# Performance work log

Hardware: AMD Instinct MI355X
Metric: run time of the kernel (lower is better)

The kernel has to match this reference:

```python
import jax, jax.numpy as jnp
import numpy as np

N_NODES = 100000
N_EDGES = 1600000
IN_DIM = 128
HID = 64


def _init_linear(key, fan_in, fan_out):
    kw, kb = jax.random.split(key)
    bound = 1.0 / np.sqrt(fan_in)
    W = jax.random.uniform(kw, (fan_in, fan_out), jnp.float32, -bound, bound)
    b = jax.random.uniform(kb, (fan_out,), jnp.float32, -bound, bound)
    return W, b


def setup_inputs() -> dict:
    key = jax.random.key(0)
    ks = jax.random.split(key, 6)
    x = jax.random.normal(ks[0], (N_NODES, IN_DIM), jnp.float32)
    edge_index = jax.random.randint(ks[1], (2, N_EDGES), 0, N_NODES, jnp.int64)
    W_pre, b_pre = _init_linear(ks[2], IN_DIM, HID)
    W1, b1 = _init_linear(ks[3], HID, HID)
    W2, b2 = _init_linear(ks[4], HID, HID)
    W3, b3 = _init_linear(ks[5], HID, HID)
    return {"x": x, "edge_index": edge_index, "W_pre": W_pre, "b_pre": b_pre,
            "W1": W1, "b1": b1, "W2": W2, "b2": b2, "W3": W3, "b3": b3}


def _gcn_layer(h, src, dst, dinv, W, b):
    # PyG GCNConv: h' = D^{-1/2} (A + I) D^{-1/2} (h W) + b, deg from A+I
    n = h.shape[0]
    hw = h @ W                                  # [N, out]
    norm = dinv[src] * dinv[dst]                # [E]
    msg = hw[src] * norm[:, None]               # gather + scale  [E, out]
    agg = jax.ops.segment_sum(msg, dst, num_segments=n)  # scatter-add
    agg = agg + hw * (dinv * dinv)[:, None]     # self-loop term (norm = dinv_i^2)
    return agg + b


def reference(x, edge_index, W_pre, b_pre, W1, b1, W2, b2, W3, b3):
    src, dst = edge_index[0], edge_index[1]
    n = x.shape[0]
    # degree of A + I (self loops added, as in GCNConv default)
    deg = jax.ops.segment_sum(jnp.ones(src.shape[0], x.dtype), dst, num_segments=n) + 1.0
    dinv = jax.lax.rsqrt(deg)

    h = x @ W_pre + b_pre                       # feature_pre linear
    h = jax.nn.relu(_gcn_layer(h, src, dst, dinv, W1, b1))  # dropout is identity in eval
    h = jax.nn.relu(_gcn_layer(h, src, dst, dinv, W2, b2))
    h = _gcn_layer(h, src, dst, dinv, W3, b3)
    # F.normalize(p=2, dim=-1) with eps=1e-12
    nrm = jnp.linalg.norm(h, axis=-1, keepdims=True)
    return h / jnp.maximum(nrm, 1e-12)
```

## Files before the change

kernel.cpp:

```cpp
#include <hip/hip_runtime.h>
#include <hip/hip_bf16.h>

#define N_NODES 100000
#define N_EDGES 1600000
#define IN_DIM 128
#define HID 64
#define NB 782

typedef __attribute__((ext_vector_type(8))) _Float16 h8v;
typedef __attribute__((ext_vector_type(4))) float f4v;

__global__ __launch_bounds__(256) void k_bhist(const int* __restrict__ dst,
                                               int* __restrict__ bsz) {
  __shared__ int cnt[NB];
  for (int b = threadIdx.x; b < NB; b += 256) cnt[b] = 0;
  __syncthreads();
  int e0 = blockIdx.x * 8192;
  int eend = min(e0 + 8192, N_EDGES);
  for (int e = e0 + threadIdx.x; e < eend; e += 256)
    atomicAdd(&cnt[dst[e] >> 7], 1);
  __syncthreads();
  for (int b = threadIdx.x; b < NB; b += 256)
    if (cnt[b]) atomicAdd(&bsz[b], cnt[b]);
}

__global__ __launch_bounds__(1024) void k_bscan(const int* __restrict__ bsz,
                                                int* __restrict__ bboff,
                                                int* __restrict__ bcur) {
  __shared__ int sc[1024];
  int t = threadIdx.x;
  int v = (t < NB) ? bsz[t] : 0;
  sc[t] = v;
  __syncthreads();
  for (int off = 1; off < 1024; off <<= 1) {
    int u = (t >= off) ? sc[t - off] : 0;
    __syncthreads();
    sc[t] += u;
    __syncthreads();
  }
  if (t < NB) {
    int excl = sc[t] - v;
    bboff[t] = excl;
    bcur[t] = excl;
    if (t == NB - 1) bboff[NB] = excl + v;
  }
}

__global__ __launch_bounds__(256) void k_partition(const int* __restrict__ ei,
                                                   int* __restrict__ bcur,
                                                   int2* __restrict__ pairs) {
  __shared__ int cnt[NB];
  __shared__ int base[NB];
  for (int b = threadIdx.x; b < NB; b += 256) cnt[b] = 0;
  __syncthreads();
  int e0 = blockIdx.x * 8192;
  int eend = min(e0 + 8192, N_EDGES);
  for (int e = e0 + threadIdx.x; e < eend; e += 256) {
    int d = ei[N_EDGES + e];
    atomicAdd(&cnt[d >> 7], 1);
  }
  __syncthreads();
  for (int b = threadIdx.x; b < NB; b += 256) {
    int c = cnt[b];
    base[b] = c ? atomicAdd(&bcur[b], c) : 0;
    cnt[b] = 0;
  }
  __syncthreads();
  for (int e = e0 + threadIdx.x; e < eend; e += 256) {
    int s = ei[e];
    int d = ei[N_EDGES + e];
    int b = d >> 7;
    int r = atomicAdd(&cnt[b], 1);
    pairs[base[b] + r] = make_int2(s, d);
  }
}

__global__ __launch_bounds__(256) void k_csr_deg(const int2* __restrict__ pairs,
                                                 const int* __restrict__ bboff,
                                                 int* __restrict__ offs,
                                                 float* __restrict__ dinv,
                                                 int* __restrict__ csr) {
  __shared__ int ldeg[128];
  __shared__ int sc[128];
  __shared__ int lcur[128];
  int t = threadIdx.x;
  int node0 = blockIdx.x << 7;
  int nloc = min(128, N_NODES - node0);
  int beg = bboff[blockIdx.x];
  int end = bboff[blockIdx.x + 1];
  if (t < 128) ldeg[t] = 0;
  __syncthreads();
  for (int i = beg + t; i < end; i += 256)
    atomicAdd(&ldeg[pairs[i].y - node0], 1);
  __syncthreads();
  int dv = (t < 128) ? ldeg[t] : 0;
  if (t < 128) sc[t] = dv;
  __syncthreads();
  for (int off = 1; off < 128; off <<= 1) {
    int u = (t >= off && t < 128) ? sc[t - off] : 0;
    __syncthreads();
    if (t < 128) sc[t] += u;
    __syncthreads();
  }
  if (t < nloc) {
    int excl = sc[t] - dv;
    int o = beg + excl;
    offs[node0 + t] = o;
    lcur[t] = o;
    dinv[node0 + t] = rsqrtf((float)dv + 1.0f);
  }
  if (blockIdx.x == NB - 1 && t == 0) offs[N_NODES] = N_EDGES;
  __syncthreads();
  for (int i = beg + t; i < end; i += 256) {
    int2 p = pairs[i];
    int pos = atomicAdd(&lcur[p.y - node0], 1);
    csr[pos] = p.x;
  }
}

__device__ __forceinline__ void split_one(const float* W, _Float16* hi, _Float16* lo,
                                          int K, int i) {
  int k = i >> 6, n = i & 63;
  float v = W[i];
  _Float16 h = (_Float16)v;
  float r = v - (float)h;
  hi[n * K + k] = h;
  lo[n * K + k] = (_Float16)r;
}

__global__ __launch_bounds__(256) void k_prep_all(
    const float* __restrict__ Wp, const float* __restrict__ W1,
    const float* __restrict__ W2, const float* __restrict__ W3,
    _Float16* __restrict__ WpH, _Float16* __restrict__ WpL,
    _Float16* __restrict__ W1H, _Float16* __restrict__ W1L,
    _Float16* __restrict__ W2H, _Float16* __restrict__ W2L,
    _Float16* __restrict__ W3H, _Float16* __restrict__ W3L) {
  int blk = blockIdx.x;
  if (blk < 32) split_one(Wp, WpH, WpL, IN_DIM, blk * 256 + threadIdx.x);
  else if (blk < 48) split_one(W1, W1H, W1L, HID, (blk - 32) * 256 + threadIdx.x);
  else if (blk < 64) split_one(W2, W2H, W2L, HID, (blk - 48) * 256 + threadIdx.x);
  else split_one(W3, W3H, W3L, HID, (blk - 64) * 256 + threadIdx.x);
}

template <int K, bool BIAS, typename OutT>
__global__ __launch_bounds__(256) void k_gemm_mfma(const float* __restrict__ X,
                                                   const _Float16* __restrict__ Wh,
                                                   const _Float16* __restrict__ Wl,
                                                   const float* __restrict__ bias,
                                                   OutT* __restrict__ out) {
  int wave = threadIdx.x >> 6;
  int lane = threadIdx.x & 63;
  int fi = lane & 15;
  int quad = lane >> 4;
  int r0 = blockIdx.x * 64 + wave * 16;
  int row_l = r0 + fi;
  if (row_l >= N_NODES) row_l = N_NODES - 1;
  const float* xp = X + (size_t)row_l * K + quad * 8;

  f4v acc[4];
#pragma unroll
  for (int ct = 0; ct < 4; ++ct) acc[ct] = (f4v){0.f, 0.f, 0.f, 0.f};

#pragma unroll
  for (int k0 = 0; k0 < K; k0 += 32) {
    f4v xa = *(const f4v*)(xp + k0);
    f4v xb = *(const f4v*)(xp + k0 + 4);
    h8v ah, al;
#pragma unroll
    for (int j = 0; j < 4; ++j) {
      _Float16 h = (_Float16)xa[j];
      ah[j] = h;
      al[j] = (_Float16)(xa[j] - (float)h);
    }
#pragma unroll
    for (int j = 0; j < 4; ++j) {
      _Float16 h = (_Float16)xb[j];
      ah[4 + j] = h;
      al[4 + j] = (_Float16)(xb[j] - (float)h);
    }
    const _Float16* whp = Wh + (size_t)fi * K + k0 + quad * 8;
    const _Float16* wlp = Wl + (size_t)fi * K + k0 + quad * 8;
#pragma unroll
    for (int ct = 0; ct < 4; ++ct) {
      h8v bh = *(const h8v*)(whp + (size_t)ct * 16 * K);
      h8v bl = *(const h8v*)(wlp + (size_t)ct * 16 * K);
      acc[ct] = __builtin_amdgcn_mfma_f32_16x16x32_f16(ah, bh, acc[ct], 0, 0, 0);
      acc[ct] = __builtin_amdgcn_mfma_f32_16x16x32_f16(al, bh, acc[ct], 0, 0, 0);
      acc[ct] = __builtin_amdgcn_mfma_f32_16x16x32_f16(ah, bl, acc[ct], 0, 0, 0);
    }
  }

#pragma unroll
  for (int ct = 0; ct < 4; ++ct) {
    float bv = 0.f;
    if (BIAS) bv = bias[ct * 16 + fi];
#pragma unroll
    for (int j = 0; j < 4; ++j) {
      int orow = r0 + quad * 4 + j;
      if (orow < N_NODES) out[(size_t)orow * HID + ct * 16 + fi] = (OutT)(acc[ct][j] + bv);
    }
  }
}

template <int MODE>
__global__ __launch_bounds__(256) void k_agg(const _Float16* __restrict__ hw,
                                             const int* __restrict__ offs,
                                             const int* __restrict__ csr,
                                             const float* __restrict__ dinv,
                                             const float* __restrict__ bias,
                                             float* __restrict__ out) {
  int node = blockIdx.x * 4 + (threadIdx.x >> 6);
  int lane = threadIdx.x & 63;
  int oct = lane >> 3;
  int fi = lane & 7;
  float di = dinv[node];
  int beg = offs[node];
  int end = offs[node + 1];

  float acc[8];
#pragma unroll
  for (int c = 0; c < 8; ++c) acc[c] = 0.f;

  if (oct == 0) {
    h8v hv = *(const h8v*)(hw + (size_t)node * HID + fi * 8);
    float w = di * di;
#pragma unroll
    for (int c = 0; c < 8; ++c) acc[c] += (float)hv[c] * w;
  }
  for (int e0 = beg + oct; e0 < end; e0 += 16) {
    int ss[2];
    float ww[2];
#pragma unroll
    for (int j = 0; j < 2; ++j) {
      int e = e0 + 8 * j;
      bool v = e < end;
      int s = csr[v ? e : beg];
      ss[j] = v ? s : node;
      ww[j] = v ? di : 0.0f;
    }
#pragma unroll
    for (int j = 0; j < 2; ++j) ww[j] *= dinv[ss[j]];
    h8v hv[2];
#pragma unroll
    for (int j = 0; j < 2; ++j)
      hv[j] = *(const h8v*)(hw + (size_t)ss[j] * HID + fi * 8);
#pragma unroll
    for (int j = 0; j < 2; ++j)
#pragma unroll
      for (int c = 0; c < 8; ++c) acc[c] += (float)hv[j][c] * ww[j];
  }
#pragma unroll
  for (int c = 0; c < 8; ++c) {
    float v = acc[c];
    v += __shfl_xor(v, 8);
    v += __shfl_xor(v, 16);
    v += __shfl_xor(v, 32);
    acc[c] = v;
  }
  if (oct == 0) {
#pragma unroll
    for (int c = 0; c < 8; ++c) acc[c] += bias[fi * 8 + c];
    if (MODE == 0) {
#pragma unroll
      for (int c = 0; c < 8; ++c) acc[c] = fmaxf(acc[c], 0.f);
    } else {
      float ss = 0.f;
#pragma unroll
      for (int c = 0; c < 8; ++c) ss += acc[c] * acc[c];
      ss += __shfl_xor(ss, 1);
      ss += __shfl_xor(ss, 2);
      ss += __shfl_xor(ss, 4);
      float sc = 1.0f / fmaxf(sqrtf(ss), 1e-12f);
#pragma unroll
      for (int c = 0; c < 8; ++c) acc[c] *= sc;
    }
    f4v o0 = {acc[0], acc[1], acc[2], acc[3]};
    f4v o1 = {acc[4], acc[5], acc[6], acc[7]};
    *(f4v*)(out + (size_t)node * HID + fi * 8) = o0;
    *(f4v*)(out + (size_t)node * HID + fi * 8 + 4) = o1;
  }
}

extern "C" void kernel_launch(void* const* d_in, const int* in_sizes, int n_in,
                              void* d_out, int out_size, void* d_ws, size_t ws_size,
                              hipStream_t stream) {
  const float* x     = (const float*)d_in[0];
  const int*   ei    = (const int*)d_in[1];
  const float* W_pre = (const float*)d_in[2];
  const float* b_pre = (const float*)d_in[3];
  const float* W1    = (const float*)d_in[4];
  const float* b1    = (const float*)d_in[5];
  const float* W2    = (const float*)d_in[6];
  const float* b2    = (const float*)d_in[7];
  const float* W3    = (const float*)d_in[8];
  const float* b3    = (const float*)d_in[9];
  float* out = (float*)d_out;

  char* ws = (char*)d_ws;
  float*    bufA  = (float*)(ws + 0);
  int2*     pairs = (int2*)(ws + 0);
  _Float16* hw16  = (_Float16*)(ws + 25600000);
  int*      csr   = (int*)(ws + 38400000);
  int*      offs  = (int*)(ws + 44800000);
  float*    dinv  = (float*)(ws + 45200016);
  int*      bsz   = (int*)(ws + 45600016);
  int*      bboff = (int*)(ws + 45603200);
  int*      bcur  = (int*)(ws + 45606400);
  _Float16* WpreH = (_Float16*)(ws + 45610000);
  _Float16* WpreL = (_Float16*)(ws + 45626384);
  _Float16* W1H   = (_Float16*)(ws + 45642768);
  _Float16* W1L   = (_Float16*)(ws + 45650960);
  _Float16* W2H   = (_Float16*)(ws + 45659152);
  _Float16* W2L   = (_Float16*)(ws + 45667344);
  _Float16* W3H   = (_Float16*)(ws + 45675536);
  _Float16* W3L   = (_Float16*)(ws + 45683728);

  const int GEMM_BLOCKS = (N_NODES + 63) / 64;
  const int PART_BLOCKS = (N_EDGES + 8191) / 8192;

  hipMemsetAsync(bsz, 0, NB * sizeof(int), stream);
  k_bhist<<<PART_BLOCKS, 256, 0, stream>>>(ei + N_EDGES, bsz);
  k_bscan<<<1, 1024, 0, stream>>>(bsz, bboff, bcur);
  k_partition<<<PART_BLOCKS, 256, 0, stream>>>(ei, bcur, pairs);
  k_csr_deg<<<NB, 256, 0, stream>>>(pairs, bboff, offs, dinv, csr);

  k_prep_all<<<80, 256, 0, stream>>>(W_pre, W1, W2, W3, WpreH, WpreL,
                                     W1H, W1L, W2H, W2L, W3H, W3L);

  k_gemm_mfma<IN_DIM, true, float><<<GEMM_BLOCKS, 256, 0, stream>>>(x, WpreH, WpreL, b_pre, bufA);

  k_gemm_mfma<HID, false, _Float16><<<GEMM_BLOCKS, 256, 0, stream>>>(bufA, W1H, W1L, nullptr, hw16);
  k_agg<0><<<N_NODES / 4, 256, 0, stream>>>(hw16, offs, csr, dinv, b1, bufA);
  k_gemm_mfma<HID, false, _Float16><<<GEMM_BLOCKS, 256, 0, stream>>>(bufA, W2H, W2L, nullptr, hw16);
  k_agg<0><<<N_NODES / 4, 256, 0, stream>>>(hw16, offs, csr, dinv, b2, bufA);
  k_gemm_mfma<HID, false, _Float16><<<GEMM_BLOCKS, 256, 0, stream>>>(bufA, W3H, W3L, nullptr, hw16);
  k_agg<1><<<N_NODES / 4, 256, 0, stream>>>(hw16, offs, csr, dinv, b3, out);
}
```

Measured before the change: 386.1 us.

## Fuse whole GCN pipeline into one cooperative persistent kernel with grid syncs

```diff
diff --git a/kernel.cpp b/kernel.cpp
--- a/kernel.cpp
+++ b/kernel.cpp
@@ -1,125 +1,44 @@
 #include <hip/hip_runtime.h>
-#include <hip/hip_bf16.h>
+#include <hip/hip_cooperative_groups.h>
+
+namespace cg = cooperative_groups;
 
 #define N_NODES 100000
 #define N_EDGES 1600000
 #define IN_DIM 128
 #define HID 64
 #define NB 782
+#define NT64 1563
+#define NGROUP 25000
+#define MAXGRID 2048
 
 typedef __attribute__((ext_vector_type(8))) _Float16 h8v;
 typedef __attribute__((ext_vector_type(4))) float f4v;
 
-__global__ __launch_bounds__(256) void k_bhist(const int* __restrict__ dst,
-                                               int* __restrict__ bsz) {
-  __shared__ int cnt[NB];
-  for (int b = threadIdx.x; b < NB; b += 256) cnt[b] = 0;
-  __syncthreads();
-  int e0 = blockIdx.x * 8192;
-  int eend = min(e0 + 8192, N_EDGES);
-  for (int e = e0 + threadIdx.x; e < eend; e += 256)
-    atomicAdd(&cnt[dst[e] >> 7], 1);
-  __syncthreads();
-  for (int b = threadIdx.x; b < NB; b += 256)
-    if (cnt[b]) atomicAdd(&bsz[b], cnt[b]);
-}
-
-__global__ __launch_bounds__(1024) void k_bscan(const int* __restrict__ bsz,
-                                                int* __restrict__ bboff,
-                                                int* __restrict__ bcur) {
-  __shared__ int sc[1024];
-  int t = threadIdx.x;
-  int v = (t < NB) ? bsz[t] : 0;
-  sc[t] = v;
-  __syncthreads();
-  for (int off = 1; off < 1024; off <<= 1) {
-    int u = (t >= off) ? sc[t - off] : 0;
-    __syncthreads();
-    sc[t] += u;
-    __syncthreads();
-  }
-  if (t < NB) {
-    int excl = sc[t] - v;
-    bboff[t] = excl;
-    bcur[t] = excl;
-    if (t == NB - 1) bboff[NB] = excl + v;
-  }
-}
-
-__global__ __launch_bounds__(256) void k_partition(const int* __restrict__ ei,
-                                                   int* __restrict__ bcur,
-                                                   int2* __restrict__ pairs) {
-  __shared__ int cnt[NB];
-  __shared__ int base[NB];
-  for (int b = threadIdx.x; b < NB; b += 256) cnt[b] = 0;
-  __syncthreads();
-  int e0 = blockIdx.x * 8192;
-  int eend = min(e0 + 8192, N_EDGES);
-  for (int e = e0 + threadIdx.x; e < eend; e += 256) {
-    int d = ei[N_EDGES + e];
-    atomicAdd(&cnt[d >> 7], 1);
-  }
-  __syncthreads();
-  for (int b = threadIdx.x; b < NB; b += 256) {
-    int c = cnt[b];
-    base[b] = c ? atomicAdd(&bcur[b], c) : 0;
-    cnt[b] = 0;
-  }
-  __syncthreads();
-  for (int e = e0 + threadIdx.x; e < eend; e += 256) {
-    int s = ei[e];
-    int d = ei[N_EDGES + e];
-    int b = d >> 7;
-    int r = atomicAdd(&cnt[b], 1);
-    pairs[base[b] + r] = make_int2(s, d);
-  }
-}
-
-__global__ __launch_bounds__(256) void k_csr_deg(const int2* __restrict__ pairs,
-                                                 const int* __restrict__ bboff,
-                                                 int* __restrict__ offs,
-                                                 float* __restrict__ dinv,
-                                                 int* __restrict__ csr) {
-  __shared__ int ldeg[128];
-  __shared__ int sc[128];
-  __shared__ int lcur[128];
-  int t = threadIdx.x;
-  int node0 = blockIdx.x << 7;
-  int nloc = min(128, N_NODES - node0);
-  int beg = bboff[blockIdx.x];
-  int end = bboff[blockIdx.x + 1];
-  if (t < 128) ldeg[t] = 0;
-  __syncthreads();
-  for (int i = beg + t; i < end; i += 256)
-    atomicAdd(&ldeg[pairs[i].y - node0], 1);
-  __syncthreads();
-  int dv = (t < 128) ? ldeg[t] : 0;
-  if (t < 128) sc[t] = dv;
-  __syncthreads();
-  for (int off = 1; off < 128; off <<= 1) {
-    int u = (t >= off && t < 128) ? sc[t - off] : 0;
-    __syncthreads();
-    if (t < 128) sc[t] += u;
-    __syncthreads();
-  }
-  if (t < nloc) {
-    int excl = sc[t] - dv;
-    int o = beg + excl;
-    offs[node0 + t] = o;
-    lcur[t] = o;
-    dinv[node0 + t] = rsqrtf((float)dv + 1.0f);
-  }
-  if (blockIdx.x == NB - 1 && t == 0) offs[N_NODES] = N_EDGES;
-  __syncthreads();
-  for (int i = beg + t; i < end; i += 256) {
-    int2 p = pairs[i];
-    int pos = atomicAdd(&lcur[p.y - node0], 1);
-    csr[pos] = p.x;
-  }
-}
-
-__device__ __forceinline__ void split_one(const float* W, _Float16* hi, _Float16* lo,
-                                          int K, int i) {
+struct MegaArgs {
+  const float* x; const int* ei;
+  const float* Wp; const float* bp;
+  const float* W1; const float* b1;
+  const float* W2; const float* b2;
+  const float* W3; const float* b3;
+  float* out;
+  float* bufA; _Float16* hw16;
+  int* pairs; int* csr; int* offs; float* dinv;
+  int* bsz; int* bboff; int* bcur;
+  _Float16* WpH; _Float16* WpL; _Float16* W1H; _Float16* W1L;
+  _Float16* W2H; _Float16* W2L; _Float16* W3H; _Float16* W3L;
+};
+
+union SM {
+  int bh[NB];
+  struct { int cnt[NB]; int base[NB]; } part;
+  struct { int ldeg[128]; int sc[128]; int lcur[128]; } cd;
+  int scan[256];
+};
+
+__device__ __forceinline__ void d_split(const float* __restrict__ W,
+                                        _Float16* __restrict__ hi,
+                                        _Float16* __restrict__ lo, int K, int i) {
   int k = i >> 6, n = i & 63;
   float v = W[i];
   _Float16 h = (_Float16)v;
@@ -128,31 +47,17 @@
   lo[n * K + k] = (_Float16)r;
 }
 
-__global__ __launch_bounds__(256) void k_prep_all(
-    const float* __restrict__ Wp, const float* __restrict__ W1,
-    const float* __restrict__ W2, const float* __restrict__ W3,
-    _Float16* __restrict__ WpH, _Float16* __restrict__ WpL,
-    _Float16* __restrict__ W1H, _Float16* __restrict__ W1L,
-    _Float16* __restrict__ W2H, _Float16* __restrict__ W2L,
-    _Float16* __restrict__ W3H, _Float16* __restrict__ W3L) {
-  int blk = blockIdx.x;
-  if (blk < 32) split_one(Wp, WpH, WpL, IN_DIM, blk * 256 + threadIdx.x);
-  else if (blk < 48) split_one(W1, W1H, W1L, HID, (blk - 32) * 256 + threadIdx.x);
-  else if (blk < 64) split_one(W2, W2H, W2L, HID, (blk - 48) * 256 + threadIdx.x);
-  else split_one(W3, W3H, W3L, HID, (blk - 64) * 256 + threadIdx.x);
-}
-
 template <int K, bool BIAS, typename OutT>
-__global__ __launch_bounds__(256) void k_gemm_mfma(const float* __restrict__ X,
-                                                   const _Float16* __restrict__ Wh,
-                                                   const _Float16* __restrict__ Wl,
-                                                   const float* __restrict__ bias,
-                                                   OutT* __restrict__ out) {
+__device__ __forceinline__ void d_gemm(int tile, const float* __restrict__ X,
+                                       const _Float16* __restrict__ Wh,
+                                       const _Float16* __restrict__ Wl,
+                                       const float* __restrict__ bias,
+                                       OutT* __restrict__ out) {
   int wave = threadIdx.x >> 6;
   int lane = threadIdx.x & 63;
   int fi = lane & 15;
   int quad = lane >> 4;
-  int r0 = blockIdx.x * 64 + wave * 16;
+  int r0 = tile * 64 + wave * 16;
   int row_l = r0 + fi;
   if (row_l >= N_NODES) row_l = N_NODES - 1;
   const float* xp = X + (size_t)row_l * K + quad * 8;
@@ -189,7 +94,6 @@
       acc[ct] = __builtin_amdgcn_mfma_f32_16x16x32_f16(ah, bl, acc[ct], 0, 0, 0);
     }
   }
-
 #pragma unroll
   for (int ct = 0; ct < 4; ++ct) {
     float bv = 0.f;
@@ -203,13 +107,13 @@
 }
 
 template <int MODE>
-__global__ __launch_bounds__(256) void k_agg(const _Float16* __restrict__ hw,
-                                             const int* __restrict__ offs,
-                                             const int* __restrict__ csr,
-                                             const float* __restrict__ dinv,
-                                             const float* __restrict__ bias,
-                                             float* __restrict__ out) {
-  int node = blockIdx.x * 4 + (threadIdx.x >> 6);
+__device__ __forceinline__ void d_agg(int grp, const _Float16* __restrict__ hw,
+                                      const int* __restrict__ offs,
+                                      const int* __restrict__ csr,
+                                      const float* __restrict__ dinv,
+                                      const float* __restrict__ bias,
+                                      float* __restrict__ out) {
+  int node = grp * 4 + (threadIdx.x >> 6);
   int lane = threadIdx.x & 63;
   int oct = lane >> 3;
   int fi = lane & 7;
@@ -227,11 +131,11 @@
 #pragma unroll
     for (int c = 0; c < 8; ++c) acc[c] += (float)hv[c] * w;
   }
-  for (int e0 = beg + oct; e0 < end; e0 += 16) {
-    int ss[2];
-    float ww[2];
-#pragma unroll
-    for (int j = 0; j < 2; ++j) {
+  for (int e0 = beg + oct; e0 < end; e0 += 32) {
+    int ss[4];
+    float ww[4];
+#pragma unroll
+    for (int j = 0; j < 4; ++j) {
       int e = e0 + 8 * j;
       bool v = e < end;
       int s = csr[v ? e : beg];
@@ -239,13 +143,13 @@
       ww[j] = v ? di : 0.0f;
     }
 #pragma unroll
-    for (int j = 0; j < 2; ++j) ww[j] *= dinv[ss[j]];
-    h8v hv[2];
-#pragma unroll
-    for (int j = 0; j < 2; ++j)
+    for (int j = 0; j < 4; ++j) ww[j] *= dinv[ss[j]];
+    h8v hv[4];
+#pragma unroll
+    for (int j = 0; j < 4; ++j)
       hv[j] = *(const h8v*)(hw + (size_t)ss[j] * HID + fi * 8);
 #pragma unroll
-    for (int j = 0; j < 2; ++j)
+    for (int j = 0; j < 4; ++j)
 #pragma unroll
       for (int c = 0; c < 8; ++c) acc[c] += (float)hv[j][c] * ww[j];
   }
@@ -281,58 +185,331 @@
   }
 }
 
+__global__ __launch_bounds__(256, 4) void k_mega(MegaArgs a) {
+  cg::grid_group g = cg::this_grid();
+  __shared__ SM sm;
+  int blk = blockIdx.x;
+  int grid = gridDim.x;
+  int t = threadIdx.x;
+
+  if (blk == 0) {
+    for (int i = t; i < NB; i += 256) a.bsz[i] = 0;
+  } else if (blk <= 32) {
+    d_split(a.Wp, a.WpH, a.WpL, IN_DIM, (blk - 1) * 256 + t);
+  } else if (blk <= 48) {
+    d_split(a.W1, a.W1H, a.W1L, HID, (blk - 33) * 256 + t);
+  } else if (blk <= 64) {
+    d_split(a.W2, a.W2H, a.W2L, HID, (blk - 49) * 256 + t);
+  } else if (blk <= 80) {
+    d_split(a.W3, a.W3H, a.W3L, HID, (blk - 65) * 256 + t);
+  }
+  g.sync();
+
+  if (blk < 196) {
+    for (int i = t; i < NB; i += 256) sm.bh[i] = 0;
+    __syncthreads();
+    int e0 = blk * 8192, e1 = min(e0 + 8192, N_EDGES);
+    for (int e = e0 + t; e < e1; e += 256)
+      atomicAdd(&sm.bh[a.ei[N_EDGES + e] >> 7], 1);
+    __syncthreads();
+    for (int i = t; i < NB; i += 256)
+      if (sm.bh[i]) atomicAdd(&a.bsz[i], sm.bh[i]);
+  } else {
+    for (int tile = blk - 196; tile < NT64; tile += grid - 196)
+      d_gemm<IN_DIM, true, float>(tile, a.x, a.WpH, a.WpL, a.bp, a.bufA);
+  }
+  g.sync();
+
+  if (blk == 0) {
+    int c[4];
+    int idx0 = t * 4;
+#pragma unroll
+    for (int j = 0; j < 4; ++j) c[j] = (idx0 + j < NB) ? a.bsz[idx0 + j] : 0;
+    int tsum = c[0] + c[1] + c[2] + c[3];
+    int val = tsum;
+    sm.scan[t] = val;
+    __syncthreads();
+    for (int off = 1; off < 256; off <<= 1) {
+      int u = (t >= off) ? sm.scan[t - off] : 0;
+      __syncthreads();
+      val += u;
+      sm.scan[t] = val;
+      __syncthreads();
+    }
+    int excl = val - tsum;
+#pragma unroll
+    for (int j = 0; j < 4; ++j) {
+      int idx = idx0 + j;
+      if (idx < NB) { a.bboff[idx] = excl; a.bcur[idx] = excl; }
+      excl += c[j];
+    }
+    if (t == 255) a.bboff[NB] = val;
+  }
+  g.sync();
+
+  if (blk < 196) {
+    for (int i = t; i < NB; i += 256) sm.part.cnt[i] = 0;
+    __syncthreads();
+    int e0 = blk * 8192, e1 = min(e0 + 8192, N_EDGES);
+    for (int e = e0 + t; e < e1; e += 256)
+      atomicAdd(&sm.part.cnt[a.ei[N_EDGES + e] >> 7], 1);
+    __syncthreads();
+    for (int i = t; i < NB; i += 256) {
+      int c = sm.part.cnt[i];
+      sm.part.base[i] = c ? atomicAdd(&a.bcur[i], c) : 0;
+      sm.part.cnt[i] = 0;
+    }
+    __syncthreads();
+    for (int e = e0 + t; e < e1; e += 256) {
+      int s = a.ei[e];
+      int d = a.ei[N_EDGES + e];
+      int b = d >> 7;
+      int r = atomicAdd(&sm.part.cnt[b], 1);
+      a.pairs[sm.part.base[b] + r] = ((d & 127) << 17) | s;
+    }
+  }
+  g.sync();
+
+  for (int b = blk; b < NB; b += grid) {
+    int node0 = b << 7;
+    int nloc = min(128, N_NODES - node0);
+    int beg = a.bboff[b], end = a.bboff[b + 1];
+    if (t < 128) sm.cd.ldeg[t] = 0;
+    __syncthreads();
+    for (int i = beg + t; i < end; i += 256)
+      atomicAdd(&sm.cd.ldeg[(a.pairs[i] >> 17) & 127], 1);
+    __syncthreads();
+    int dv = (t < 128) ? sm.cd.ldeg[t] : 0;
+    if (t < 128) sm.cd.sc[t] = dv;
+    __syncthreads();
+    for (int off = 1; off < 128; off <<= 1) {
+      int u = (t >= off && t < 128) ? sm.cd.sc[t - off] : 0;
+      __syncthreads();
+      if (t < 128) sm.cd.sc[t] += u;
+      __syncthreads();
+    }
+    if (t < nloc) {
+      int o = beg + sm.cd.sc[t] - dv;
+      a.offs[node0 + t] = o;
+      sm.cd.lcur[t] = o;
+      a.dinv[node0 + t] = rsqrtf((float)dv + 1.0f);
+    }
+    if (b == NB - 1 && t == 0) a.offs[N_NODES] = N_EDGES;
+    __syncthreads();
+    for (int i = beg + t; i < end; i += 256) {
+      int p = a.pairs[i];
+      int pos = atomicAdd(&sm.cd.lcur[(p >> 17) & 127], 1);
+      a.csr[pos] = p & 131071;
+    }
+    __syncthreads();
+  }
+  g.sync();
+
+  for (int tile = blk; tile < NT64; tile += grid)
+    d_gemm<HID, false, _Float16>(tile, a.bufA, a.W1H, a.W1L, nullptr, a.hw16);
+  g.sync();
+  for (int grp = blk; grp < NGROUP; grp += grid)
+    d_agg<0>(grp, a.hw16, a.offs, a.csr, a.dinv, a.b1, a.bufA);
+  g.sync();
+
+  for (int tile = blk; tile < NT64; tile += grid)
+    d_gemm<HID, false, _Float16>(tile, a.bufA, a.W2H, a.W2L, nullptr, a.hw16);
+  g.sync();
+  for (int grp = blk; grp < NGROUP; grp += grid)
+    d_agg<0>(grp, a.hw16, a.offs, a.csr, a.dinv, a.b2, a.bufA);
+  g.sync();
+
+  for (int tile = blk; tile < NT64; tile += grid)
+    d_gemm<HID, false, _Float16>(tile, a.bufA, a.W3H, a.W3L, nullptr, a.hw16);
+  g.sync();
+  for (int grp = blk; grp < NGROUP; grp += grid)
+    d_agg<1>(grp, a.hw16, a.offs, a.csr, a.dinv, a.b3, a.out);
+}
+
+__global__ __launch_bounds__(256) void f_prep(MegaArgs a) {
+  int blk = blockIdx.x, t = threadIdx.x;
+  if (blk < 32) d_split(a.Wp, a.WpH, a.WpL, IN_DIM, blk * 256 + t);
+  else if (blk < 48) d_split(a.W1, a.W1H, a.W1L, HID, (blk - 32) * 256 + t);
+  else if (blk < 64) d_split(a.W2, a.W2H, a.W2L, HID, (blk - 48) * 256 + t);
+  else d_split(a.W3, a.W3H, a.W3L, HID, (blk - 64) * 256 + t);
+}
+
+__global__ __launch_bounds__(256) void f_bhist(MegaArgs a) {
+  __shared__ int cnt[NB];
+  int t = threadIdx.x;
+  for (int i = t; i < NB; i += 256) cnt[i] = 0;
+  __syncthreads();
+  int e0 = blockIdx.x * 8192, e1 = min(e0 + 8192, N_EDGES);
+  for (int e = e0 + t; e < e1; e += 256)
+    atomicAdd(&cnt[a.ei[N_EDGES + e] >> 7], 1);
+  __syncthreads();
+  for (int i = t; i < NB; i += 256)
+    if (cnt[i]) atomicAdd(&a.bsz[i], cnt[i]);
+}
+
+__global__ __launch_bounds__(256) void f_bscan(MegaArgs a) {
+  __shared__ int sm[256];
+  int t = threadIdx.x;
+  int c[4];
+  int idx0 = t * 4;
+#pragma unroll
+  for (int j = 0; j < 4; ++j) c[j] = (idx0 + j < NB) ? a.bsz[idx0 + j] : 0;
+  int tsum = c[0] + c[1] + c[2] + c[3];
+  int val = tsum;
+  sm[t] = val;
+  __syncthreads();
+  for (int off = 1; off < 256; off <<= 1) {
+    int u = (t >= off) ? sm[t - off] : 0;
+    __syncthreads();
+    val += u;
+    sm[t] = val;
+    __syncthreads();
+  }
+  int excl = val - tsum;
+#pragma unroll
+  for (int j = 0; j < 4; ++j) {
+    int idx = idx0 + j;
+    if (idx < NB) { a.bboff[idx] = excl; a.bcur[idx] = excl; }
+    excl += c[j];
+  }
+  if (t == 255) a.bboff[NB] = val;
+}
+
+__global__ __launch_bounds__(256) void f_partition(MegaArgs a) {
+  __shared__ int cnt[NB];
+  __shared__ int base[NB];
+  int t = threadIdx.x;
+  for (int i = t; i < NB; i += 256) cnt[i] = 0;
+  __syncthreads();
+  int e0 = blockIdx.x * 8192, e1 = min(e0 + 8192, N_EDGES);
+  for (int e = e0 + t; e < e1; e += 256)
+    atomicAdd(&cnt[a.ei[N_EDGES + e] >> 7], 1);
+  __syncthreads();
+  for (int i = t; i < NB; i += 256) {
+    int c = cnt[i];
+    base[i] = c ? atomicAdd(&a.bcur[i], c) : 0;
+    cnt[i] = 0;
+  }
+  __syncthreads();
+  for (int e = e0 + t; e < e1; e += 256) {
+    int s = a.ei[e];
+    int d = a.ei[N_EDGES + e];
+    int b = d >> 7;
+    int r = atomicAdd(&cnt[b], 1);
+    a.pairs[base[b] + r] = ((d & 127) << 17) | s;
+  }
+}
+
+__global__ __launch_bounds__(256) void f_csrdeg(MegaArgs a) {
+  __shared__ int ldeg[128];
+  __shared__ int sc[128];
+  __shared__ int lcur[128];
+  int t = threadIdx.x;
+  int b = blockIdx.x;
+  int node0 = b << 7;
+  int nloc = min(128, N_NODES - node0);
+  int beg = a.bboff[b], end = a.bboff[b + 1];
+  if (t < 128) ldeg[t] = 0;
+  __syncthreads();
+  for (int i = beg + t; i < end; i += 256)
+    atomicAdd(&ldeg[(a.pairs[i] >> 17) & 127], 1);
+  __syncthreads();
+  int dv = (t < 128) ? ldeg[t] : 0;
+  if (t < 128) sc[t] = dv;
+  __syncthreads();
+  for (int off = 1; off < 128; off <<= 1) {
+    int u = (t >= off && t < 128) ? sc[t - off] : 0;
+    __syncthreads();
+    if (t < 128) sc[t] += u;
+    __syncthreads();
+  }
+  if (t < nloc) {
+    int o = beg + sc[t] - dv;
+    a.offs[node0 + t] = o;
+    lcur[t] = o;
+    a.dinv[node0 + t] = rsqrtf((float)dv + 1.0f);
+  }
+  if (b == NB - 1 && t == 0) a.offs[N_NODES] = N_EDGES;
+  __syncthreads();
+  for (int i = beg + t; i < end; i += 256) {
+    int p = a.pairs[i];
+    int pos = atomicAdd(&lcur[(p >> 17) & 127], 1);
+    a.csr[pos] = p & 131071;
+  }
+}
+
+__global__ __launch_bounds__(256) void f_gemm_pre(MegaArgs a) {
+  d_gemm<IN_DIM, true, float>(blockIdx.x, a.x, a.WpH, a.WpL, a.bp, a.bufA);
+}
+
+__global__ __launch_bounds__(256) void f_gemm64(MegaArgs a, const _Float16* Wh,
+                                                const _Float16* Wl) {
+  d_gemm<HID, false, _Float16>(blockIdx.x, a.bufA, Wh, Wl, nullptr, a.hw16);
+}
+
+__global__ __launch_bounds__(256) void f_agg_relu(MegaArgs a, const float* bias) {
+  d_agg<0>(blockIdx.x, a.hw16, a.offs, a.csr, a.dinv, bias, a.bufA);
+}
+
+__global__ __launch_bounds__(256) void f_agg_norm(MegaArgs a) {
+  d_agg<1>(blockIdx.x, a.hw16, a.offs, a.csr, a.dinv, a.b3, a.out);
+}
+
 extern "C" void kernel_launch(void* const* d_in, const int* in_sizes, int n_in,
                               void* d_out, int out_size, void* d_ws, size_t ws_size,
                               hipStream_t stream) {
-  const float* x     = (const float*)d_in[0];
-  const int*   ei    = (const int*)d_in[1];
-  const float* W_pre = (const float*)d_in[2];
-  const float* b_pre = (const float*)d_in[3];
-  const float* W1    = (const float*)d_in[4];
-  const float* b1    = (const float*)d_in[5];
-  const float* W2    = (const float*)d_in[6];
-  const float* b2    = (const float*)d_in[7];
-  const float* W3    = (const float*)d_in[8];
-  const float* b3    = (const float*)d_in[9];
-  float* out = (float*)d_out;
-
   char* ws = (char*)d_ws;
-  float*    bufA  = (float*)(ws + 0);
-  int2*     pairs = (int2*)(ws + 0);
-  _Float16* hw16  = (_Float16*)(ws + 25600000);
-  int*      csr   = (int*)(ws + 38400000);
-  int*      offs  = (int*)(ws + 44800000);
-  float*    dinv  = (float*)(ws + 45200016);
-  int*      bsz   = (int*)(ws + 45600016);
-  int*      bboff = (int*)(ws + 45603200);
-  int*      bcur  = (int*)(ws + 45606400);
-  _Float16* WpreH = (_Float16*)(ws + 45610000);
-  _Float16* WpreL = (_Float16*)(ws + 45626384);
-  _Float16* W1H   = (_Float16*)(ws + 45642768);
-  _Float16* W1L   = (_Float16*)(ws + 45650960);
-  _Float16* W2H   = (_Float16*)(ws + 45659152);
-  _Float16* W2L   = (_Float16*)(ws + 45667344);
-  _Float16* W3H   = (_Float16*)(ws + 45675536);
-  _Float16* W3L   = (_Float16*)(ws + 45683728);
-
-  const int GEMM_BLOCKS = (N_NODES + 63) / 64;
-  const int PART_BLOCKS = (N_EDGES + 8191) / 8192;
-
-  hipMemsetAsync(bsz, 0, NB * sizeof(int), stream);
-  k_bhist<<<PART_BLOCKS, 256, 0, stream>>>(ei + N_EDGES, bsz);
-  k_bscan<<<1, 1024, 0, stream>>>(bsz, bboff, bcur);
-  k_partition<<<PART_BLOCKS, 256, 0, stream>>>(ei, bcur, pairs);
-  k_csr_deg<<<NB, 256, 0, stream>>>(pairs, bboff, offs, dinv, csr);
-
-  k_prep_all<<<80, 256, 0, stream>>>(W_pre, W1, W2, W3, WpreH, WpreL,
-                                     W1H, W1L, W2H, W2L, W3H, W3L);
-
-  k_gemm_mfma<IN_DIM, true, float><<<GEMM_BLOCKS, 256, 0, stream>>>(x, WpreH, WpreL, b_pre, bufA);
-
-  k_gemm_mfma<HID, false, _Float16><<<GEMM_BLOCKS, 256, 0, stream>>>(bufA, W1H, W1L, nullptr, hw16);
-  k_agg<0><<<N_NODES / 4, 256, 0, stream>>>(hw16, offs, csr, dinv, b1, bufA);
-  k_gemm_mfma<HID, false, _Float16><<<GEMM_BLOCKS, 256, 0, stream>>>(bufA, W2H, W2L, nullptr, hw16);
-  k_agg<0><<<N_NODES / 4, 256, 0, stream>>>(hw16, offs, csr, dinv, b2, bufA);
-  k_gemm_mfma<HID, false, _Float16><<<GEMM_BLOCKS, 256, 0, stream>>>(bufA, W3H, W3L, nullptr, hw16);
-  k_agg<1><<<N_NODES / 4, 256, 0, stream>>>(hw16, offs, csr, dinv, b3, out);
-}
+  MegaArgs a;
+  a.x  = (const float*)d_in[0];
+  a.ei = (const int*)d_in[1];
+  a.Wp = (const float*)d_in[2];  a.bp = (const float*)d_in[3];
+  a.W1 = (const float*)d_in[4];  a.b1 = (const float*)d_in[5];
+  a.W2 = (const float*)d_in[6];  a.b2 = (const float*)d_in[7];
+  a.W3 = (const float*)d_in[8];  a.b3 = (const float*)d_in[9];
+  a.out  = (float*)d_out;
+  a.bufA = (float*)(ws + 0);
+  a.hw16 = (_Float16*)(ws + 25600000);
+  a.pairs = (int*)(ws + 38400000);
+  a.csr   = (int*)(ws + 44800000);
+  a.offs  = (int*)(ws + 51200000);
+  a.dinv  = (float*)(ws + 51600016);
+  a.bsz   = (int*)(ws + 52000016);
+  a.bboff = (int*)(ws + 52003152);
+  a.bcur  = (int*)(ws + 52006288);
+  a.WpH = (_Float16*)(ws + 52009424);
+  a.WpL = (_Float16*)(ws + 52025808);
+  a.W1H = (_Float16*)(ws + 52042192);
+  a.W1L = (_Float16*)(ws + 52050384);
+  a.W2H = (_Float16*)(ws + 52058576);
+  a.W2L = (_Float16*)(ws + 52066768);
+  a.W3H = (_Float16*)(ws + 52074960);
+  a.W3L = (_Float16*)(ws + 52083152);
+
+  int per_cu = 0;
+  hipError_t qerr = hipOccupancyMaxActiveBlocksPerMultiprocessor(
+      &per_cu, (const void*)k_mega, 256, 0);
+  int grid = (qerr == hipSuccess) ? per_cu * 256 : 0;
+  if (grid > MAXGRID) grid = MAXGRID;
+
+  hipError_t lerr = hipErrorUnknown;
+  if (grid >= 256) {
+    void* params[] = {(void*)&a};
+    lerr = hipLaunchCooperativeKernel((const void*)k_mega, dim3(grid), dim3(256),
+                                      params, 0, stream);
+  }
+  if (lerr != hipSuccess) {
+    (void)hipMemsetAsync(a.bsz, 0, NB * sizeof(int), stream);
+    f_prep<<<80, 256, 0, stream>>>(a);
+    f_bhist<<<196, 256, 0, stream>>>(a);
+    f_bscan<<<1, 256, 0, stream>>>(a);
+    f_partition<<<196, 256, 0, stream>>>(a);
+    f_csrdeg<<<NB, 256, 0, stream>>>(a);
+    f_gemm_pre<<<NT64, 256, 0, stream>>>(a);
+    f_gemm64<<<NT64, 256, 0, stream>>>(a, a.W1H, a.W1L);
+    f_agg_relu<<<NGROUP, 256, 0, stream>>>(a, a.b1);
+    f_gemm64<<<NT64, 256, 0, stream>>>(a, a.W2H, a.W2L);
+    f_agg_relu<<<NGROUP, 256, 0, stream>>>(a, a.b2);
+    f_gemm64<<<NT64, 256, 0, stream>>>(a, a.W3H, a.W3L);
+    f_agg_norm<<<NGROUP, 256, 0, stream>>>(a);
+  }
+}
```

Result: slower. 1.121 ms (+190.3%).
